# Optimization experiments

Measured on AMD Instinct MI355X. Metric: run time of the kernel, lower is better.

## Reference

```python
import jax, jax.numpy as jnp
import numpy as np

D_MODEL = 1024
D_INNER = 4096
N_EXPERTS = 8
TOP_K = 2
B, S = 4, 2048


def setup_inputs() -> dict:
    key = jax.random.key(0)
    ks = jax.random.split(key, 7)
    s_d = 1.0 / np.sqrt(D_MODEL)
    s_h = 1.0 / np.sqrt(D_INNER)
    return {
        "x": jax.random.normal(ks[0], (B, S, D_MODEL), dtype=jnp.float32),
        "router_w": jax.random.normal(ks[1], (N_EXPERTS, D_MODEL), dtype=jnp.float32) * s_d,
        "router_b": jnp.zeros((N_EXPERTS,), dtype=jnp.float32),
        "gate_w": jax.random.normal(ks[2], (N_EXPERTS, D_INNER, D_MODEL), dtype=jnp.float32) * s_d,
        "up_w": jax.random.normal(ks[3], (N_EXPERTS, D_INNER, D_MODEL), dtype=jnp.float32) * s_d,
        "down_w": jax.random.normal(ks[4], (N_EXPERTS, D_MODEL, D_INNER), dtype=jnp.float32) * s_h,
    }


def reference(x, router_w, router_b, gate_w, up_w, down_w):
    # Router: softmax over experts, top-k, renormalize.
    logits = jnp.einsum('bsd,ed->bse', x, router_w) + router_b
    probs = jax.nn.softmax(logits, axis=-1)
    topk_p, topk_i = jax.lax.top_k(probs, TOP_K)            # [B,S,K]
    topk_p = topk_p / jnp.sum(topk_p, axis=-1, keepdims=True)
    # Per-expert combine weight: [B,S,E] (zero for unselected experts).
    onehot = jax.nn.one_hot(topk_i, N_EXPERTS, dtype=x.dtype)  # [B,S,K,E]
    cw = jnp.einsum('bsk,bske->bse', topk_p, onehot)
    # Loop over the small fixed set of experts; weighted combine.
    out = jnp.zeros_like(x)
    for e in range(N_EXPERTS):
        g = jnp.einsum('bsd,hd->bsh', x, gate_w[e])
        u = jnp.einsum('bsd,hd->bsh', x, up_w[e])
        h = jax.nn.silu(g) * u
        y = jnp.einsum('bsh,dh->bsd', h, down_w[e])
        out = out + cw[..., e:e + 1] * y
    return out
```

## Files before the change

kernel.cpp:

```cpp
#include <hip/hip_runtime.h>


#define DM 1024
#define DI 4096
#define NE 8
#define TOK 8192
#define MAXPE 8192
#define NT2 72

typedef __attribute__((ext_vector_type(4))) float f32x4;
typedef __attribute__((ext_vector_type(8))) short bf16x8;
typedef __attribute__((ext_vector_type(8))) unsigned short u16x8;

#define MFMA(a, b, c) __builtin_amdgcn_mfma_f32_16x16x32_bf16(a, b, c, 0, 0, 0)
#define GLDS16(g, l) __builtin_amdgcn_global_load_lds( \
    (const __attribute__((address_space(1))) unsigned int*)(g), \
    (__attribute__((address_space(3))) unsigned int*)(l), 16, 0, 0)

__device__ __forceinline__ unsigned short bf16_rn(float f) {
    unsigned int u = __builtin_bit_cast(unsigned int, f);
    u += 0x7fffu + ((u >> 16) & 1u);
    return (unsigned short)(u >> 16);
}

__global__ __launch_bounds__(256) void router_kernel(
    const float* __restrict__ x, const float* __restrict__ rw,
    const float* __restrict__ rb,
    int* __restrict__ counts, int* __restrict__ tok_list,
    float* __restrict__ w_list)
{
    int t = blockIdx.x * 4 + (threadIdx.x >> 6);
    int lane = threadIdx.x & 63;
    const float* xr = x + (size_t)t * DM;
    float acc[NE];
#pragma unroll
    for (int e = 0; e < NE; ++e) acc[e] = 0.f;
    for (int i = lane; i < DM; i += 64) {
        float xv = xr[i];
#pragma unroll
        for (int e = 0; e < NE; ++e) acc[e] += xv * rw[e * DM + i];
    }
#pragma unroll
    for (int e = 0; e < NE; ++e) {
        float v = acc[e];
#pragma unroll
        for (int s = 32; s >= 1; s >>= 1) v += __shfl_xor(v, s, 64);
        acc[e] = v;
    }
    if (lane == 0) {
        float l0 = -3.4e38f, l1 = -3.4e38f;
        int i0 = 0, i1 = 0;
#pragma unroll
        for (int e = 0; e < NE; ++e) {
            float v = acc[e] + rb[e];
            if (v > l0) { l1 = l0; i1 = i0; l0 = v; i0 = e; }
            else if (v > l1) { l1 = v; i1 = e; }
        }
        float z = expf(l1 - l0);
        float w0 = 1.f / (1.f + z);
        float w1 = z / (1.f + z);
        int p0 = atomicAdd(&counts[i0], 1);
        tok_list[i0 * MAXPE + p0] = t; w_list[i0 * MAXPE + p0] = w0;
        int p1 = atomicAdd(&counts[i1], 1);
        tok_list[i1 * MAXPE + p1] = t; w_list[i1 * MAXPE + p1] = w1;
    }
}

__global__ void scan_kernel(const int* __restrict__ counts,
                            int* __restrict__ offs, int* __restrict__ tiles2) {
    if (threadIdx.x == 0) {
        int s = 0, nt = 0;
        for (int e = 0; e < NE; ++e) { offs[e] = s; s += counts[e]; }
        for (int e = 0; e < NE; ++e) {
            int nmb = (counts[e] + 255) / 256;
            for (int mb = 0; mb < nmb && nt < NT2; ++mb)
                tiles2[nt++] = (e << 16) | mb;
        }
        for (; nt < NT2; ++nt) tiles2[nt] = -1;
    }
}

__global__ __launch_bounds__(256) void conv_kernel(
    const float* __restrict__ src, unsigned short* __restrict__ dst,
    long total, int shift, long estride)
{
    long i8 = ((long)blockIdx.x * 256 + threadIdx.x) * 8;
    if (i8 >= total) return;
    long e = i8 >> shift;
    long r = i8 - (e << shift);
    const float* s = src + e * estride + r;
    f32x4 a = *(const f32x4*)s;
    f32x4 b = *(const f32x4*)(s + 4);
    u16x8 o;
#pragma unroll
    for (int j = 0; j < 4; ++j) { o[j] = bf16_rn(a[j]); o[4 + j] = bf16_rn(b[j]); }
    *(u16x8*)(dst + i8) = o;
}

#define STAGEX(LDS_, SRC0_, SRC1_, H_, ST_) do { if ((ST_) < NKT) { \
    GLDS16((SRC0_) + (size_t)(ST_) * 64, &LDS_[(ST_) & 1][H_][w * 512]); \
    GLDS16((SRC1_) + (size_t)(ST_) * 64, &LDS_[(ST_) & 1][H_][(8 + w) * 512]); } } while (0)

#define PHASE(BUFI, RH, CH, STMT) do { \
    bf16x8 a_[4][2], b_[2][2]; \
    _Pragma("unroll") for (int mf = 0; mf < 4; ++mf) \
    _Pragma("unroll") for (int kk = 0; kk < 2; ++kk) \
        a_[mf][kk] = *(const bf16x8*)((const char*)&ldsA[BUFI][RH][0] + \
            (wm * 64 + mf * 16 + lr) * 128 + ((kk * 64 + lk * 16) ^ xsw)); \
    _Pragma("unroll") for (int nf = 0; nf < 2; ++nf) \
    _Pragma("unroll") for (int kk = 0; kk < 2; ++kk) \
        b_[nf][kk] = *(const bf16x8*)((const char*)&ldsB[BUFI][CH][0] + \
            (wn * 32 + nf * 16 + lr) * 128 + ((kk * 64 + lk * 16) ^ xsw)); \
    STMT; \
    __builtin_amdgcn_sched_barrier(0); \
    __builtin_amdgcn_s_barrier(); \
    asm volatile("s_waitcnt lgkmcnt(0)" ::: "memory"); \
    __builtin_amdgcn_sched_barrier(0); \
    __builtin_amdgcn_s_setprio(1); \
    _Pragma("unroll") for (int mf = 0; mf < 4; ++mf) \
    _Pragma("unroll") for (int nf = 0; nf < 2; ++nf) \
    _Pragma("unroll") for (int kk = 0; kk < 2; ++kk) \
        acc[(RH) * 4 + mf][(CH) * 2 + nf] = \
            MFMA(a_[mf][kk], b_[nf][kk], acc[(RH) * 4 + mf][(CH) * 2 + nf]); \
    __builtin_amdgcn_s_setprio(0); \
    __builtin_amdgcn_sched_barrier(0); \
    __builtin_amdgcn_s_barrier(); \
} while (0)

#define VMW4 do { asm volatile("s_waitcnt vmcnt(4)" ::: "memory"); \
                  __builtin_amdgcn_sched_barrier(0); } while (0)

__global__ __launch_bounds__(512, 2) void gateup8(
    const unsigned short* __restrict__ xb,
    const unsigned short* __restrict__ gwb,
    const unsigned short* __restrict__ uwb,
    const int* __restrict__ counts, const int* __restrict__ offs,
    const int* __restrict__ tiles2, const int* __restrict__ tok_list,
    unsigned short* __restrict__ H, int cb, int CHC)
{
    const int tx = ((blockIdx.x & 7) * 9) + (blockIdx.x >> 3);
    const int pk = tiles2[tx];
    if (pk < 0) return;
    const int e = pk >> 16, tile = pk & 0xffff;
    const int ne = counts[e];
    const int by = blockIdx.y;
    const int tid = threadIdx.x, lane = tid & 63, w = tid >> 6;
    const int lr = lane & 15, lk = lane >> 4;
    const int wm = w >> 2, wn = w & 3;
    const int xsw = (lr & 7) << 4;
    const int NKT = DM / 64;
    const int NIT = NKT / 2;

    __shared__ __align__(16) unsigned short ldsA[2][2][8192];
    __shared__ __align__(16) unsigned short ldsB[2][2][8192];

    const unsigned short* sA[2][2];
    const unsigned short* sB[2][2];
#pragma unroll
    for (int q = 0; q < 2; ++q)
#pragma unroll
        for (int h = 0; h < 2; ++h) {
            int bi = q * 8 + w;
            int l8 = bi * 8 + (lane >> 3);
            int scol = (((lane & 7) ^ (l8 & 7)) << 3);
            int R = ((l8 >> 6) << 7) | (h << 6) | (l8 & 63);
            int rg = tile * 256 + R;
            int rc = rg < ne ? rg : ne - 1;
            int tok = tok_list[e * MAXPE + rc];
            sA[q][h] = xb + (size_t)tok * DM + scol;
            int cc = ((l8 >> 5) << 6) | (h << 5) | (l8 & 31);
            int br = by * 256 + cc;
            int mat = (cc >> 4) & 1;
            int wrow = ((br >> 5) << 4) + (br & 15);
            const unsigned short* pB = mat ? uwb : gwb;
            sB[q][h] = pB + ((size_t)e * CHC + wrow) * DM + scol;
        }

    f32x4 acc[8][4];
#pragma unroll
    for (int m = 0; m < 8; ++m)
#pragma unroll
        for (int n = 0; n < 4; ++n) acc[m][n] = (f32x4)0.f;

    STAGEX(ldsA, sA[0][0], sA[1][0], 0, 0);
    STAGEX(ldsB, sB[0][0], sB[1][0], 0, 0);
    STAGEX(ldsA, sA[0][1], sA[1][1], 1, 0);
    STAGEX(ldsB, sB[0][1], sB[1][1], 1, 0);
    STAGEX(ldsA, sA[0][0], sA[1][0], 0, 1);
    STAGEX(ldsB, sB[0][0], sB[1][0], 0, 1);
    VMW4;
    __builtin_amdgcn_s_barrier();

#pragma unroll 1
    for (int i = 0; i < NIT; ++i) {
        const int t1 = 2 * i + 1;
        PHASE(0, 0, 0, STAGEX(ldsA, sA[0][1], sA[1][1], 1, t1));
        PHASE(0, 0, 1, STAGEX(ldsB, sB[0][1], sB[1][1], 1, t1));
        PHASE(0, 1, 0, STAGEX(ldsA, sA[0][0], sA[1][0], 0, t1 + 1));
        PHASE(0, 1, 1, STAGEX(ldsB, sB[0][0], sB[1][0], 0, t1 + 1));
        VMW4;
        PHASE(1, 0, 0, STAGEX(ldsA, sA[0][1], sA[1][1], 1, t1 + 1));
        PHASE(1, 0, 1, STAGEX(ldsB, sB[0][1], sB[1][1], 1, t1 + 1));
        PHASE(1, 1, 0, STAGEX(ldsA, sA[0][0], sA[1][0], 0, t1 + 2));
        PHASE(1, 1, 1, STAGEX(ldsB, sB[0][0], sB[1][0], 0, t1 + 2));
        VMW4;
    }

    const int hrow0 = offs[e] + tile * 256;
#pragma unroll
    for (int am = 0; am < 8; ++am)
#pragma unroll
        for (int j = 0; j < 4; ++j) {
            int R = wm * 128 + (am >> 2) * 64 + (am & 3) * 16 + lk * 4 + j;
            if (tile * 256 + R < ne) {
#pragma unroll
                for (int ch = 0; ch < 2; ++ch) {
                    float g = acc[am][ch * 2 + 0][j];
                    float u = acc[am][ch * 2 + 1][j];
                    float hv = (g / (1.f + expf(-g))) * u;
                    int brb = by * 256 + wn * 64 + ch * 32 + lr;
                    int hcol = cb + ((brb >> 5) << 4) + (brb & 15);
                    H[(size_t)(hrow0 + R) * DI + hcol] = bf16_rn(hv);
                }
            }
        }
}

__global__ __launch_bounds__(512, 2) void down8(
    const unsigned short* __restrict__ dwb,
    const int* __restrict__ counts, const int* __restrict__ offs,
    const int* __restrict__ tiles2, const int* __restrict__ tok_list,
    const float* __restrict__ w_list,
    const unsigned short* __restrict__ H,
    float* __restrict__ out)
{
    const int tx = ((blockIdx.x & 7) * 9) + (blockIdx.x >> 3);
    const int pk = tiles2[tx];
    if (pk < 0) return;
    const int e = pk >> 16, tile = pk & 0xffff;
    const int ne = counts[e];
    const int by = blockIdx.y >> 1;
    const int kq = blockIdx.y & 1;
    const int tid = threadIdx.x, lane = tid & 63, w = tid >> 6;
    const int lr = lane & 15, lk = lane >> 4;
    const int wm = w >> 2, wn = w & 3;
    const int xsw = (lr & 7) << 4;
    const int NKT = (DI / 2) / 64;
    const int NIT = NKT / 2;
    const int kbase = kq * (DI / 2);

    __shared__ __align__(16) unsigned short ldsA[2][2][8192];
    __shared__ __align__(16) unsigned short ldsB[2][2][8192];

    const int hrow0 = offs[e] + tile * 256;
    const unsigned short* sA[2][2];
    const unsigned short* sB[2][2];
#pragma unroll
    for (int q = 0; q < 2; ++q)
#pragma unroll
        for (int h = 0; h < 2; ++h) {
            int bi = q * 8 + w;
            int l8 = bi * 8 + (lane >> 3);
            int scol = (((lane & 7) ^ (l8 & 7)) << 3);
            int R = ((l8 >> 6) << 7) | (h << 6) | (l8 & 63);
            sA[q][h] = H + (size_t)(hrow0 + R) * DI + kbase + scol;
            int cc = ((l8 >> 5) << 6) | (h << 5) | (l8 & 31);
            sB[q][h] = dwb + ((size_t)e * DM + by * 256 + cc) * DI + kbase + scol;
        }

    f32x4 acc[8][4];
#pragma unroll
    for (int m = 0; m < 8; ++m)
#pragma unroll
        for (int n = 0; n < 4; ++n) acc[m][n] = (f32x4)0.f;

    STAGEX(ldsA, sA[0][0], sA[1][0], 0, 0);
    STAGEX(ldsB, sB[0][0], sB[1][0], 0, 0);
    STAGEX(ldsA, sA[0][1], sA[1][1], 1, 0);
    STAGEX(ldsB, sB[0][1], sB[1][1], 1, 0);
    STAGEX(ldsA, sA[0][0], sA[1][0], 0, 1);
    STAGEX(ldsB, sB[0][0], sB[1][0], 0, 1);
    VMW4;
    __builtin_amdgcn_s_barrier();

#pragma unroll 1
    for (int i = 0; i < NIT; ++i) {
        const int t1 = 2 * i + 1;
        PHASE(0, 0, 0, STAGEX(ldsA, sA[0][1], sA[1][1], 1, t1));
        PHASE(0, 0, 1, STAGEX(ldsB, sB[0][1], sB[1][1], 1, t1));
        PHASE(0, 1, 0, STAGEX(ldsA, sA[0][0], sA[1][0], 0, t1 + 1));
        PHASE(0, 1, 1, STAGEX(ldsB, sB[0][0], sB[1][0], 0, t1 + 1));
        VMW4;
        PHASE(1, 0, 0, STAGEX(ldsA, sA[0][1], sA[1][1], 1, t1 + 1));
        PHASE(1, 0, 1, STAGEX(ldsB, sB[0][1], sB[1][1], 1, t1 + 1));
        PHASE(1, 1, 0, STAGEX(ldsA, sA[0][0], sA[1][0], 0, t1 + 2));
        PHASE(1, 1, 1, STAGEX(ldsB, sB[0][0], sB[1][0], 0, t1 + 2));
        VMW4;
    }

#pragma unroll
    for (int am = 0; am < 8; ++am)
#pragma unroll
        for (int j = 0; j < 4; ++j) {
            int R = wm * 128 + (am >> 2) * 64 + (am & 3) * 16 + lk * 4 + j;
            int grow = tile * 256 + R;
            if (grow < ne) {
                int t = tok_list[e * MAXPE + grow];
                float wgt = w_list[e * MAXPE + grow];
#pragma unroll
                for (int an = 0; an < 4; ++an) {
                    int c = by * 256 + wn * 64 + (an >> 1) * 32 + (an & 1) * 16 + lr;
                    atomicAdd(&out[(size_t)t * DM + c], wgt * acc[am][an][j]);
                }
            }
        }
}

extern "C" void kernel_launch(void* const* d_in, const int* in_sizes, int n_in,
                              void* d_out, int out_size, void* d_ws, size_t ws_size,
                              hipStream_t stream) {
    const float* x = (const float*)d_in[0];
    const float* router_w = (const float*)d_in[1];
    const float* router_b = (const float*)d_in[2];
    const float* gate_w = (const float*)d_in[3];
    const float* up_w = (const float*)d_in[4];
    const float* down_w = (const float*)d_in[5];
    float* out = (float*)d_out;

    char* ws = (char*)d_ws;
    int* counts = (int*)ws;
    int* offs = (int*)(ws + 64);
    int* tiles2 = (int*)(ws + 128);
    int* tok_list = (int*)(ws + 512);
    float* w_list = (float*)(ws + 512 + (size_t)NE * MAXPE * 4);
    size_t off = 512 + (size_t)NE * MAXPE * 8;
    off = (off + 255) & ~(size_t)255;

    unsigned short* xb = (unsigned short*)(ws + off);  off += (size_t)TOK * DM * 2;
    unsigned short* dwb = (unsigned short*)(ws + off); off += (size_t)NE * DM * DI * 2;
    unsigned short* H = (unsigned short*)(ws + off);   off += (size_t)(2 * TOK + 256) * DI * 2;

    int CHC = 128;
    for (int c = 2048; c >= 128; c >>= 1)
        if (off + (size_t)2 * NE * c * DM * 2 <= ws_size) { CHC = c; break; }
    unsigned short* gwb = (unsigned short*)(ws + off);
    unsigned short* uwb = gwb + (size_t)NE * CHC * DM;

    hipMemsetAsync(out, 0, (size_t)out_size * sizeof(float), stream);
    hipMemsetAsync(counts, 0, NE * sizeof(int), stream);

    router_kernel<<<TOK / 4, 256, 0, stream>>>(x, router_w, router_b,
                                               counts, tok_list, w_list);
    scan_kernel<<<1, 64, 0, stream>>>(counts, offs, tiles2);

    conv_kernel<<<(TOK * DM) / 2048, 256, 0, stream>>>(
        x, xb, (long)TOK * DM, 23, 0);
    conv_kernel<<<(int)(((long)NE * DM * DI) / 2048), 256, 0, stream>>>(
        down_w, dwb, (long)NE * DM * DI, 25, 0);

    const int sh = 10 + __builtin_ctz((unsigned)CHC);
    for (int cb = 0; cb < DI; cb += CHC) {
        long tot = (long)NE * CHC * DM;
        conv_kernel<<<(int)(tot / 2048), 256, 0, stream>>>(
            gate_w + (size_t)cb * DM, gwb, tot, sh, (long)DI * DM);
        conv_kernel<<<(int)(tot / 2048), 256, 0, stream>>>(
            up_w + (size_t)cb * DM, uwb, tot, sh, (long)DI * DM);
        gateup8<<<dim3(NT2, 2 * CHC / 256), 512, 0, stream>>>(
            xb, gwb, uwb, counts, offs, tiles2, tok_list, H, cb, CHC);
    }
    down8<<<dim3(NT2, 8), 512, 0, stream>>>(
        dwb, counts, offs, tiles2, tok_list, w_list, H, out);
}
```

Before: 1.030 ms.

## Replace double-buffered phased GEMM pipeline with single-buffer per-k-tile loop

```diff
diff --git a/kernel.cpp b/kernel.cpp
--- a/kernel.cpp
+++ b/kernel.cpp
@@ -97,40 +97,46 @@
     *(u16x8*)(dst + i8) = o;
 }
 
-#define STAGEX(LDS_, SRC0_, SRC1_, H_, ST_) do { if ((ST_) < NKT) { \
-    GLDS16((SRC0_) + (size_t)(ST_) * 64, &LDS_[(ST_) & 1][H_][w * 512]); \
-    GLDS16((SRC1_) + (size_t)(ST_) * 64, &LDS_[(ST_) & 1][H_][(8 + w) * 512]); } } while (0)
-
-#define PHASE(BUFI, RH, CH, STMT) do { \
-    bf16x8 a_[4][2], b_[2][2]; \
+#define STAGE1(LDS_, SRC0_, SRC1_, H_, KB_) do { \
+    GLDS16((SRC0_) + (KB_), &LDS_[H_][w * 512]); \
+    GLDS16((SRC1_) + (KB_), &LDS_[H_][(8 + w) * 512]); } while (0)
+
+#define DSA(DST_, RH) \
     _Pragma("unroll") for (int mf = 0; mf < 4; ++mf) \
     _Pragma("unroll") for (int kk = 0; kk < 2; ++kk) \
-        a_[mf][kk] = *(const bf16x8*)((const char*)&ldsA[BUFI][RH][0] + \
-            (wm * 64 + mf * 16 + lr) * 128 + ((kk * 64 + lk * 16) ^ xsw)); \
+        DST_[mf][kk] = *(const bf16x8*)((const char*)&ldsA[RH][0] + \
+            (wm * 64 + mf * 16 + lr) * 128 + ((kk * 64 + lk * 16) ^ xsw));
+
+#define DSB(DST_, CH) \
     _Pragma("unroll") for (int nf = 0; nf < 2; ++nf) \
     _Pragma("unroll") for (int kk = 0; kk < 2; ++kk) \
-        b_[nf][kk] = *(const bf16x8*)((const char*)&ldsB[BUFI][CH][0] + \
-            (wn * 32 + nf * 16 + lr) * 128 + ((kk * 64 + lk * 16) ^ xsw)); \
-    STMT; \
-    __builtin_amdgcn_sched_barrier(0); \
-    __builtin_amdgcn_s_barrier(); \
-    asm volatile("s_waitcnt lgkmcnt(0)" ::: "memory"); \
-    __builtin_amdgcn_sched_barrier(0); \
-    __builtin_amdgcn_s_setprio(1); \
+        DST_[nf][kk] = *(const bf16x8*)((const char*)&ldsB[CH][0] + \
+            (wn * 32 + nf * 16 + lr) * 128 + ((kk * 64 + lk * 16) ^ xsw));
+
+#define MFMAQ(AR_, BR_, RH, CH) \
     _Pragma("unroll") for (int mf = 0; mf < 4; ++mf) \
     _Pragma("unroll") for (int nf = 0; nf < 2; ++nf) \
     _Pragma("unroll") for (int kk = 0; kk < 2; ++kk) \
         acc[(RH) * 4 + mf][(CH) * 2 + nf] = \
-            MFMA(a_[mf][kk], b_[nf][kk], acc[(RH) * 4 + mf][(CH) * 2 + nf]); \
-    __builtin_amdgcn_s_setprio(0); \
-    __builtin_amdgcn_sched_barrier(0); \
-    __builtin_amdgcn_s_barrier(); \
+            MFMA(AR_[mf][kk], BR_[nf][kk], acc[(RH) * 4 + mf][(CH) * 2 + nf]);
+
+#define KTILE_BODY(KB_) do { \
+    STAGE1(ldsA, sA[0][0], sA[1][0], 0, KB_); \
+    STAGE1(ldsA, sA[0][1], sA[1][1], 1, KB_); \
+    STAGE1(ldsB, sB[0][0], sB[1][0], 0, KB_); \
+    STAGE1(ldsB, sB[0][1], sB[1][1], 1, KB_); \
+    __syncthreads(); \
+    DSA(ar, 0); DSB(b0r, 0); \
+    MFMAQ(ar, b0r, 0, 0); \
+    DSB(b1r, 1); \
+    MFMAQ(ar, b1r, 0, 1); \
+    DSA(ar, 1); \
+    MFMAQ(ar, b1r, 1, 1); \
+    MFMAQ(ar, b0r, 1, 0); \
+    __syncthreads(); \
 } while (0)
 
-#define VMW4 do { asm volatile("s_waitcnt vmcnt(4)" ::: "memory"); \
-                  __builtin_amdgcn_sched_barrier(0); } while (0)
-
-__global__ __launch_bounds__(512, 2) void gateup8(
+__global__ __launch_bounds__(512, 2) void gateup10(
     const unsigned short* __restrict__ xb,
     const unsigned short* __restrict__ gwb,
     const unsigned short* __restrict__ uwb,
@@ -148,11 +154,9 @@
     const int lr = lane & 15, lk = lane >> 4;
     const int wm = w >> 2, wn = w & 3;
     const int xsw = (lr & 7) << 4;
-    const int NKT = DM / 64;
-    const int NIT = NKT / 2;
-
-    __shared__ __align__(16) unsigned short ldsA[2][2][8192];
-    __shared__ __align__(16) unsigned short ldsB[2][2][8192];
+
+    __shared__ __align__(16) unsigned short ldsA[2][8192];
+    __shared__ __align__(16) unsigned short ldsB[2][8192];
 
     const unsigned short* sA[2][2];
     const unsigned short* sB[2][2];
@@ -182,28 +186,12 @@
 #pragma unroll
         for (int n = 0; n < 4; ++n) acc[m][n] = (f32x4)0.f;
 
-    STAGEX(ldsA, sA[0][0], sA[1][0], 0, 0);
-    STAGEX(ldsB, sB[0][0], sB[1][0], 0, 0);
-    STAGEX(ldsA, sA[0][1], sA[1][1], 1, 0);
-    STAGEX(ldsB, sB[0][1], sB[1][1], 1, 0);
-    STAGEX(ldsA, sA[0][0], sA[1][0], 0, 1);
-    STAGEX(ldsB, sB[0][0], sB[1][0], 0, 1);
-    VMW4;
-    __builtin_amdgcn_s_barrier();
+    bf16x8 ar[4][2], b0r[2][2], b1r[2][2];
 
 #pragma unroll 1
-    for (int i = 0; i < NIT; ++i) {
-        const int t1 = 2 * i + 1;
-        PHASE(0, 0, 0, STAGEX(ldsA, sA[0][1], sA[1][1], 1, t1));
-        PHASE(0, 0, 1, STAGEX(ldsB, sB[0][1], sB[1][1], 1, t1));
-        PHASE(0, 1, 0, STAGEX(ldsA, sA[0][0], sA[1][0], 0, t1 + 1));
-        PHASE(0, 1, 1, STAGEX(ldsB, sB[0][0], sB[1][0], 0, t1 + 1));
-        VMW4;
-        PHASE(1, 0, 0, STAGEX(ldsA, sA[0][1], sA[1][1], 1, t1 + 1));
-        PHASE(1, 0, 1, STAGEX(ldsB, sB[0][1], sB[1][1], 1, t1 + 1));
-        PHASE(1, 1, 0, STAGEX(ldsA, sA[0][0], sA[1][0], 0, t1 + 2));
-        PHASE(1, 1, 1, STAGEX(ldsB, sB[0][0], sB[1][0], 0, t1 + 2));
-        VMW4;
+    for (int kt = 0; kt < DM / 64; ++kt) {
+        const size_t kb = (size_t)kt * 64;
+        KTILE_BODY(kb);
     }
 
     const int hrow0 = offs[e] + tile * 256;
@@ -226,7 +214,7 @@
         }
 }
 
-__global__ __launch_bounds__(512, 2) void down8(
+__global__ __launch_bounds__(512, 2) void down10(
     const unsigned short* __restrict__ dwb,
     const int* __restrict__ counts, const int* __restrict__ offs,
     const int* __restrict__ tiles2, const int* __restrict__ tok_list,
@@ -245,12 +233,10 @@
     const int lr = lane & 15, lk = lane >> 4;
     const int wm = w >> 2, wn = w & 3;
     const int xsw = (lr & 7) << 4;
-    const int NKT = (DI / 2) / 64;
-    const int NIT = NKT / 2;
     const int kbase = kq * (DI / 2);
 
-    __shared__ __align__(16) unsigned short ldsA[2][2][8192];
-    __shared__ __align__(16) unsigned short ldsB[2][2][8192];
+    __shared__ __align__(16) unsigned short ldsA[2][8192];
+    __shared__ __align__(16) unsigned short ldsB[2][8192];
 
     const int hrow0 = offs[e] + tile * 256;
     const unsigned short* sA[2][2];
@@ -274,28 +260,12 @@
 #pragma unroll
         for (int n = 0; n < 4; ++n) acc[m][n] = (f32x4)0.f;
 
-    STAGEX(ldsA, sA[0][0], sA[1][0], 0, 0);
-    STAGEX(ldsB, sB[0][0], sB[1][0], 0, 0);
-    STAGEX(ldsA, sA[0][1], sA[1][1], 1, 0);
-    STAGEX(ldsB, sB[0][1], sB[1][1], 1, 0);
-    STAGEX(ldsA, sA[0][0], sA[1][0], 0, 1);
-    STAGEX(ldsB, sB[0][0], sB[1][0], 0, 1);
-    VMW4;
-    __builtin_amdgcn_s_barrier();
+    bf16x8 ar[4][2], b0r[2][2], b1r[2][2];
 
 #pragma unroll 1
-    for (int i = 0; i < NIT; ++i) {
-        const int t1 = 2 * i + 1;
-        PHASE(0, 0, 0, STAGEX(ldsA, sA[0][1], sA[1][1], 1, t1));
-        PHASE(0, 0, 1, STAGEX(ldsB, sB[0][1], sB[1][1], 1, t1));
-        PHASE(0, 1, 0, STAGEX(ldsA, sA[0][0], sA[1][0], 0, t1 + 1));
-        PHASE(0, 1, 1, STAGEX(ldsB, sB[0][0], sB[1][0], 0, t1 + 1));
-        VMW4;
-        PHASE(1, 0, 0, STAGEX(ldsA, sA[0][1], sA[1][1], 1, t1 + 1));
-        PHASE(1, 0, 1, STAGEX(ldsB, sB[0][1], sB[1][1], 1, t1 + 1));
-        PHASE(1, 1, 0, STAGEX(ldsA, sA[0][0], sA[1][0], 0, t1 + 2));
-        PHASE(1, 1, 1, STAGEX(ldsB, sB[0][0], sB[1][0], 0, t1 + 2));
-        VMW4;
+    for (int kt = 0; kt < (DI / 2) / 64; ++kt) {
+        const size_t kb = (size_t)kt * 64;
+        KTILE_BODY(kb);
     }
 
 #pragma unroll
@@ -365,9 +335,9 @@
             gate_w + (size_t)cb * DM, gwb, tot, sh, (long)DI * DM);
         conv_kernel<<<(int)(tot / 2048), 256, 0, stream>>>(
             up_w + (size_t)cb * DM, uwb, tot, sh, (long)DI * DM);
-        gateup8<<<dim3(NT2, 2 * CHC / 256), 512, 0, stream>>>(
+        gateup10<<<dim3(NT2, 2 * CHC / 256), 512, 0, stream>>>(
             xb, gwb, uwb, counts, offs, tiles2, tok_list, H, cb, CHC);
     }
-    down8<<<dim3(NT2, 8), 512, 0, stream>>>(
+    down10<<<dim3(NT2, 8), 512, 0, stream>>>(
         dwb, counts, offs, tiles2, tok_list, w_list, H, out);
 }
```

Result: no change. 1.028 ms (-0.2%).
